# Optimization experiments

Measured on AMD Instinct MI355X. Metric: run time of the kernel, lower is better.

The kernel has to match this reference:

```python
import jax, jax.numpy as jnp
import numpy as np

B, TIN, TOUT = 64, 256, 400
NM, BF = 80, 512
MID, H, PRE = BF // 4, 2 * BF, BF // 2
LOC_F, LOC_K = 32, 31


def lstm_cell(x, h, c, Wih, Whh, bih, bhh):
    gates = x @ Wih.T + bih + h @ Whh.T + bhh
    i, f, g, o = jnp.split(gates, 4, axis=-1)
    c2 = jax.nn.sigmoid(f) * c + jax.nn.sigmoid(i) * jnp.tanh(g)
    h2 = jax.nn.sigmoid(o) * jnp.tanh(c2)
    return h2, c2


def setup_inputs() -> dict:
    key = jax.random.key(0)
    ks = jax.random.split(key, 24)
    def p(k, shape, fan_in):
        return jax.random.normal(k, shape, jnp.float32) / np.sqrt(fan_in)
    return {
        'input': jax.random.normal(ks[0], (B, TIN, BF), jnp.float32),
        'input_mask': jnp.ones((B, TIN), jnp.bool_),
        'target': jax.random.normal(ks[1], (B, NM, TOUT), jnp.float32),
        'W_pre1': p(ks[2], (PRE, NM), NM), 'b_pre1': jnp.zeros((PRE,), jnp.float32),
        'W_pre2': p(ks[3], (PRE, PRE), PRE), 'b_pre2': jnp.zeros((PRE,), jnp.float32),
        'Wq': p(ks[4], (MID, H), H),
        'Wk': p(ks[5], (MID, BF), BF),
        'loc_conv': p(ks[6], (LOC_F, 2, LOC_K), 2 * LOC_K),
        'Wloc': p(ks[7], (MID, LOC_F), LOC_F),
        'v_att': p(ks[8], (MID,), MID),
        'Wih1': p(ks[9], (4 * H, BF + PRE), BF + PRE), 'Whh1': p(ks[10], (4 * H, H), H),
        'bih1': jnp.zeros((4 * H,), jnp.float32), 'bhh1': jnp.zeros((4 * H,), jnp.float32),
        'Wih2': p(ks[11], (4 * H, BF + H), BF + H), 'Whh2': p(ks[12], (4 * H, H), H),
        'bih2': jnp.zeros((4 * H,), jnp.float32), 'bhh2': jnp.zeros((4 * H,), jnp.float32),
        'Wout': p(ks[13], (NM, BF + H), BF + H), 'bout': jnp.zeros((NM,), jnp.float32),
    }


def reference(input, input_mask, target, W_pre1, b_pre1, W_pre2, b_pre2, Wq, Wk,
              loc_conv, Wloc, v_att, Wih1, Whh1, bih1, bhh1, Wih2, Whh2, bih2, bhh2,
              Wout, bout):
    b, tin, f = input.shape
    nm, tout = target.shape[1], target.shape[2]
    # teacher-forcing shift: prepend zero frame, drop last
    tgt = jnp.concatenate([jnp.zeros((b, nm, 1), target.dtype), target[:, :, :-1]], 2)
    # PreNet: two 1x1 convs (== per-channel linears) + ReLU (dropout = eval identity)
    x = jax.nn.relu(jnp.einsum('bct,oc->bot', tgt, W_pre1) + b_pre1[None, :, None])
    x = jax.nn.relu(jnp.einsum('bct,oc->bot', x, W_pre2) + b_pre2[None, :, None])  # [B,PRE,Tout]
    key_proj = jnp.einsum('btf,mf->btm', input, Wk)  # [B,Tin,MID]
    pad = (LOC_K - 1) // 2

    def step(carry, xt):
        h1, c1, h2, c2, context, aw, awc = carry
        h1, c1 = lstm_cell(jnp.concatenate([xt, context], 1), h1, c1, Wih1, Whh1, bih1, bhh1)
        # location-sensitive attention
        wpair = jnp.stack([aw, awc], 1)  # [B,2,Tin]
        loc = jax.lax.conv_general_dilated(wpair, loc_conv, (1,), [(pad, pad)],
                                           dimension_numbers=('NCH', 'OIH', 'NCH'))
        loc_feat = jnp.einsum('bct,mc->btm', loc, Wloc)
        q = h1 @ Wq.T  # [B,MID]
        e = jnp.tanh(q[:, None, :] + key_proj + loc_feat) @ v_att  # [B,Tin]
        e = jnp.where(input_mask, e, jnp.float32(-1e9))
        aw2 = jax.nn.softmax(e, axis=1)
        context2 = jnp.einsum('bt,btf->bf', aw2, input)
        awc2 = awc + aw2
        h2, c2 = lstm_cell(jnp.concatenate([h1, context2], 1), h2, c2, Wih2, Whh2, bih2, bhh2)
        out = jnp.concatenate([h2, context2], 1) @ Wout.T + bout
        return (h1, c1, h2, c2, context2, aw2, awc2), (out, aw2)

    z = lambda *s: jnp.zeros(s, input.dtype)
    carry0 = (z(b, H), z(b, H), z(b, H), z(b, H), z(b, f), z(b, tin), z(b, tin))
    xs = jnp.transpose(x, (2, 0, 1))  # [Tout,B,PRE]
    _, (outs, aws) = jax.lax.scan(step, carry0, xs)
    output = jnp.moveaxis(outs, 0, 2)  # [B,NM,Tout]
    weight = jnp.moveaxis(aws, 0, 2)   # [B,Tin,Tout]
    return output, weight
```

## Files before the change

kernel.cpp:

```cpp
#include <hip/hip_runtime.h>

#define NB 256
#define NT 512
#define DYNB 158496
#define SCOPE __HIP_MEMORY_SCOPE_AGENT

typedef __attribute__((ext_vector_type(8))) short short8;
typedef __attribute__((ext_vector_type(4))) float f32x4;

__device__ __forceinline__ float b2f(unsigned short s){ return __uint_as_float(((unsigned)s)<<16); }
__device__ __forceinline__ unsigned short f2b(float f){
  unsigned u = __float_as_uint(f);
  return (unsigned short)((u + 0x7FFFu + ((u>>16)&1u))>>16);
}
__device__ __forceinline__ float sigm(float x){ return 1.0f/(1.0f+__expf(-x)); }
__device__ __forceinline__ float tanh_(float x){ float e=__expf(-2.0f*x); return (1.0f-e)/(1.0f+e); }
__device__ __forceinline__ f32x4 mfma16(short8 a, short8 b, f32x4 c){
  return __builtin_amdgcn_mfma_f32_16x16x32_bf16(a,b,c,0,0,0);
}

__device__ __forceinline__ unsigned long long ldu64(const void* p){
  return __hip_atomic_load((const unsigned long long*)p, __ATOMIC_RELAXED, SCOPE);
}
__device__ __forceinline__ short8 ld8h(const unsigned short* p){
  union{ unsigned long long u[2]; short8 s; } r;
  r.u[0]=ldu64(p); r.u[1]=ldu64(p+4);
  return r.s;
}
__device__ __forceinline__ float2 ld2f(const float* p){
  union{ unsigned long long u; float2 f; } r; r.u=ldu64(p); return r.f;
}
__device__ __forceinline__ float ldf(const float* p){
  return __hip_atomic_load((float*)p, __ATOMIC_RELAXED, SCOPE);
}
__device__ __forceinline__ void stf(float* p, float v){
  __hip_atomic_store(p, v, __ATOMIC_RELAXED, SCOPE);
}
__device__ __forceinline__ void sth(unsigned short* p, unsigned short v){
  __hip_atomic_store(p, v, __ATOMIC_RELAXED, SCOPE);
}

__device__ __forceinline__ void gbar2(unsigned* arrive, unsigned* root, unsigned* release,
                                      int grp, unsigned& ph){
  __syncthreads();
  if (threadIdx.x==0){
    ph += 1;
    asm volatile("s_waitcnt vmcnt(0)" ::: "memory");
    unsigned old = __hip_atomic_fetch_add(&arrive[grp*32], 1u, __ATOMIC_RELAXED, SCOPE);
    if (old == ph*32u - 1u){
      __hip_atomic_fetch_add(root, 1u, __ATOMIC_RELAXED, SCOPE);
      while (__hip_atomic_load(root, __ATOMIC_RELAXED, SCOPE) < ph*8u){
        __builtin_amdgcn_s_sleep(1);
      }
      __hip_atomic_store(&release[grp*32], ph, __ATOMIC_RELAXED, SCOPE);
    } else {
      while (__hip_atomic_load(&release[grp*32], __ATOMIC_RELAXED, SCOPE) < ph){
        __builtin_amdgcn_s_sleep(1);
      }
    }
  }
  __syncthreads();
}


__global__ void maskdet_k(const unsigned* __restrict__ m32, int* __restrict__ flag){
  __shared__ int ok;
  if (threadIdx.x==0) ok = 1;
  __syncthreads();
  for (int i=threadIdx.x; i<4096; i+=256){
    if (m32[i] > 1u) ok = 0;
  }
  __syncthreads();
  if (threadIdx.x==0) *flag = ok;
}

__global__ void xin2bf_k(const float* __restrict__ xin, unsigned short* __restrict__ xinh){
  size_t i = (size_t)blockIdx.x*256 + threadIdx.x;
  if (i < (size_t)64*256*512) xinh[i] = f2b(xin[i]);
}

__global__ void prenet_k(const float* __restrict__ target, const float* __restrict__ W1, const float* __restrict__ b1,
                         const float* __restrict__ W2, const float* __restrict__ b2,
                         unsigned short* __restrict__ xbh){
  int t = blockIdx.x;
  int tid = threadIdx.x;
  __shared__ float stgt[64][80];
  __shared__ float smid[64][256];
  for(int i=tid;i<64*80;i+=256){
    int b=i/80, c=i%80;
    stgt[b][c] = (t==0)?0.f : target[((size_t)b*80+c)*400 + (t-1)];
  }
  __syncthreads();
  {
    float w1r[80];
    #pragma unroll
    for(int c=0;c<80;c++) w1r[c] = W1[tid*80+c];
    float bb1 = b1[tid];
    for(int b0=0;b0<64;b0+=16){
      float acc[16];
      #pragma unroll
      for(int i=0;i<16;i++) acc[i]=0.f;
      for(int c=0;c<80;c++){
        float wv=w1r[c];
        #pragma unroll
        for(int i=0;i<16;i++) acc[i] += wv*stgt[b0+i][c];
      }
      #pragma unroll
      for(int i=0;i<16;i++) smid[b0+i][tid] = fmaxf(acc[i]+bb1, 0.f);
    }
  }
  __syncthreads();
  {
    float bb2 = b2[tid];
    for(int b0=0;b0<64;b0+=16){
      float acc[16];
      #pragma unroll
      for(int i=0;i<16;i++) acc[i]=0.f;
      for(int c=0;c<256;c++){
        float wv=W2[tid*256+c];
        #pragma unroll
        for(int i=0;i<16;i++) acc[i] += wv*smid[b0+i][c];
      }
      #pragma unroll
      for(int i=0;i<16;i++){
        float v = fmaxf(acc[i]+bb2,0.f);
        xbh[((size_t)t*64 + b0+i)*256 + tid] = f2b(v);
      }
    }
  }
}

__global__ void keyproj_k(const float* __restrict__ xin, const float* __restrict__ Wk, unsigned short* __restrict__ keypT){
  int b = blockIdx.x>>4; int t0=(blockIdx.x&15)*16; int m=threadIdx.x;
  __shared__ float sx[16][512];
  for(int i=m;i<16*512;i+=128){ int tt=i>>9, f=i&511; sx[tt][f]=xin[((size_t)b*256+t0+tt)*512+f]; }
  __syncthreads();
  float s[16];
  #pragma unroll
  for(int i=0;i<16;i++) s[i]=0.f;
  for(int f=0;f<512;f++){
    float wv = Wk[m*512+f];
    #pragma unroll
    for(int i=0;i<16;i++) s[i]+=sx[i][f]*wv;
  }
  #pragma unroll
  for(int i=0;i<16;i++) keypT[((size_t)b*128+m)*256 + t0+i] = f2b(s[i]);
}

__global__ void prep_k(const float* bih1,const float* bhh1,const float* bih2,const float* bhh2,
                       float* bsum1,float* bsum2){
  int i0 = blockIdx.x*blockDim.x + threadIdx.x;
  int n = gridDim.x*blockDim.x;
  for(int k=i0;k<4096;k+=n){ bsum1[k]=bih1[k]+bhh1[k]; bsum2[k]=bih2[k]+bhh2[k]; }
}

__global__ void perm_k(const float* __restrict__ Wih1, const float* __restrict__ Whh1,
                       const float* __restrict__ Wih2, const float* __restrict__ Whh2,
                       unsigned short* __restrict__ Wp1h, unsigned short* __restrict__ Wp2h){
  size_t i0 = (size_t)blockIdx.x*blockDim.x + threadIdx.x;
  size_t n  = (size_t)gridDim.x*blockDim.x;
  const size_t N1 = (size_t)256*56*512;
  for(size_t idx=i0; idx<N1; idx+=n){
    int beta = (int)(idx/28672);
    int r = (int)(idx%28672);
    int kt = r/512;
    int l  = (r>>3)&63;
    int i8 = r&7;
    int c = l&15, cci = l>>4;
    int k = kt*32 + cci*8 + i8;
    int rowp = (c>>2)*1024 + beta*4 + (c&3);
    float v = (k<768)? Wih1[(size_t)rowp*768 + k] : Whh1[(size_t)rowp*1024 + (k-768)];
    Wp1h[idx] = f2b(v);
  }
  const size_t N2 = (size_t)256*80*512;
  for(size_t idx=i0; idx<N2; idx+=n){
    int beta = (int)(idx/40960);
    int r = (int)(idx%40960);
    int kt = r/512;
    int l  = (r>>3)&63;
    int i8 = r&7;
    int c = l&15, cci = l>>4;
    int k = kt*32 + cci*8 + i8;
    int rowp = (c>>2)*1024 + beta*4 + (c&3);
    float v = (k<1536)? Wih2[(size_t)rowp*1536 + k] : Whh2[(size_t)rowp*1024 + (k-1536)];
    Wp2h[idx] = f2b(v);
  }
}


struct SArgs {
  const float* xin; const float* loc_conv; const float* Wloc; const float* v_att; const float* bout;
  const float* Wq; const float* Wout;
  const unsigned short* keypT; const unsigned short* xinh;
  const unsigned short* xbh;
  const unsigned short* Wp1h; const unsigned short* Wp2h;
  const float* bsum1; const float* bsum2;
  const unsigned char* mask8; const int* mask32; const int* mflag;
  unsigned short* h1h; float* h1f;
  unsigned short* h2h; float* h2f;
  unsigned short* ctxh; float* ctxf;
  float* c1; float* c2;
  float* aw; float* awc; float* eP; float* locT;
  unsigned* arrive; unsigned* root; unsigned* release;
  float* outp; float* wout;
};

__global__ void __launch_bounds__(NT) scan_kernel(SArgs a){
  extern __shared__ char dynsm[];
  unsigned short* Lw1 = (unsigned short*)dynsm;
  unsigned short* Lw2 = (unsigned short*)(dynsm + 57344);
  float* gsc1 = (float*)(dynsm + 139264);
  float* gsc2 = (float*)(dynsm + 143616);
  float* sA   = (float*)(dynsm + 147968);
  float* sq   = (float*)(dynsm + 158208);
  float* sv   = (float*)(dynsm + 158336);
  float* red  = (float*)(dynsm + 158464);

  const int beta = ((blockIdx.x & 7) << 5) | (blockIdx.x >> 3);
  const int grp  = blockIdx.x & 7;
  const int tid = threadIdx.x;
  const int wav = tid>>6;
  const int lan = tid&63;

  const int cc  = lan>>4;
  const int b4  = beta>>2;
  const int q4  = beta&3;
  unsigned ph = 0;

  {
    const short8* g1 = (const short8*)(a.Wp1h + (size_t)beta*28672);
    short8* l1 = (short8*)Lw1;
    for (int i=tid; i<3584; i+=NT) l1[i] = g1[i];
    const short8* g2 = (const short8*)(a.Wp2h + (size_t)beta*40960);
    short8* l2 = (short8*)Lw2;
    for (int i=tid; i<5120; i+=NT) l2[i] = g2[i];
  }

  bool mv = false;
  if (tid<256) mv = (a.mflag[0] ? (a.mask32[b4*256+tid] != 0) : (a.mask8[b4*256+tid] != 0));
  __syncthreads();

  for (int tau=0; tau<=400; ++tau){
    const int p = tau&1;
    if (tau<400 && wav<4){
      const int row = wav*16 + (lan&15);
      f32x4 A0={0.f,0.f,0.f,0.f};
      const unsigned short* wh = Lw1 + lan*8;
      {
        const unsigned short* xh = a.xbh + ((size_t)tau*64 + row)*256 + cc*8;
        #pragma unroll
        for(int kt=0;kt<8;kt++)
          A0=mfma16(*(const short8*)(xh+kt*32), *(const short8*)(wh+kt*512), A0);
      }
      {
        const unsigned short* xh = a.ctxh + row*512 + cc*8;
        #pragma unroll 8
        for(int kt=8;kt<24;kt++)
          A0=mfma16(ld8h(xh+(kt-8)*32), *(const short8*)(wh+kt*512), A0);
      }
      {
        const unsigned short* xh = a.h1h + (size_t)(p^1)*65536 + row*1024 + cc*8;
        #pragma unroll 8
        for(int kt=24;kt<56;kt++)
          A0=mfma16(ld8h(xh+(kt-24)*32), *(const short8*)(wh+kt*512), A0);
      }
      #pragma unroll
      for(int r=0;r<4;r++) gsc1[(wav*16 + cc*4 + r)*17 + (lan&15)] = A0[r];
    }
    if (tau>0 && wav>=4){
      const int wv2 = wav-4;
      const int row = wv2*16 + (lan&15);
      f32x4 A0={0.f,0.f,0.f,0.f};
      const unsigned short* wh = Lw2 + lan*8;
      {
        const unsigned short* xh = a.h1h + (size_t)(p^1)*65536 + row*1024 + cc*8;
        #pragma unroll 8
        for(int kt=0;kt<32;kt++)
          A0=mfma16(ld8h(xh+kt*32), *(const short8*)(wh+kt*512), A0);
      }
      {
        const unsigned short* xh = a.ctxh + row*512 + cc*8;
        #pragma unroll 8
        for(int kt=32;kt<48;kt++)
          A0=mfma16(ld8h(xh+(kt-32)*32), *(const short8*)(wh+kt*512), A0);
      }
      {
        const unsigned short* xh = a.h2h + (size_t)p*65536 + row*1024 + cc*8;
        #pragma unroll 8
        for(int kt=48;kt<80;kt++)
          A0=mfma16(ld8h(xh+(kt-48)*32), *(const short8*)(wh+kt*512), A0);
      }
      #pragma unroll
      for(int r=0;r<4;r++) gsc2[(wv2*16 + cc*4 + r)*17 + (lan&15)] = A0[r];
    }
    __syncthreads();
    if (tau<400 && tid<256){
      int m = tid>>2, j = tid&3, u = beta*4+j;
      float gi = gsc1[m*17+0+j]  + a.bsum1[0*1024+u];
      float gf = gsc1[m*17+4+j]  + a.bsum1[1*1024+u];
      float gg = gsc1[m*17+8+j]  + a.bsum1[2*1024+u];
      float go = gsc1[m*17+12+j] + a.bsum1[3*1024+u];
      float cp = a.c1[m*1024+u];
      float cn = sigm(gf)*cp + sigm(gi)*tanh_(gg);
      a.c1[m*1024+u] = cn;
      float hn = sigm(go)*tanh_(cn);
      stf(a.h1f + m*1024+u, hn);
      sth(a.h1h + (size_t)p*65536 + m*1024 + u, f2b(hn));
    }
    if (tau>0 && tid>=256){
      int t2 = tid-256;
      int m = t2>>2, j = t2&3, u = beta*4+j;
      float gi = gsc2[m*17+0+j]  + a.bsum2[0*1024+u];
      float gf = gsc2[m*17+4+j]  + a.bsum2[1*1024+u];
      float gg = gsc2[m*17+8+j]  + a.bsum2[2*1024+u];
      float go = gsc2[m*17+12+j] + a.bsum2[3*1024+u];
      float cp = a.c2[m*1024+u];
      float cn = sigm(gf)*cp + sigm(gi)*tanh_(gg);
      a.c2[m*1024+u] = cn;
      float hn = sigm(go)*tanh_(cn);
      stf(a.h2f + m*1024+u, hn);
      sth(a.h2h + (size_t)(p^1)*65536 + m*1024 + u, f2b(hn));
    }
    if (tau<400){
      if (tid<128){
        float2 v = ld2f(a.aw + b4*256 + tid*2);
        sA[tid*2]=v.x; sA[tid*2+1]=v.y;
        float2 w2 = ld2f(a.awc + b4*256 + tid*2);
        sA[256+tid*2]=w2.x; sA[257+tid*2]=w2.y;
      }
      for(int i=tid;i<1984;i+=NT) sA[512+i] = a.loc_conv[i];
    }
    __syncthreads();
    if (tau<400){
      const int t0 = q4*64;
      #pragma unroll
      for(int jj=0;jj<4;jj++){
        int o = tid*4+jj;
        int f = o>>6, tl = o&63, t = t0+tl;
        float s = 0.f;
        #pragma unroll
        for(int c=0;c<2;c++){
          const float* kw = &sA[512 + (f*2+c)*31];
          const float* wv = &sA[c*256];
          for(int k=0;k<31;k++){
            int tt = t + k - 15;
            if (tt>=0 && tt<256) s += wv[tt]*kw[k];
          }
        }
        stf(a.locT + (size_t)b4*8192 + f*256 + t, s);
      }
    }
    gbar2(a.arrive, a.root, a.release, grp, ph);
    if (tau<400 && tid<256){
      for(int i=tid*2;i<1024;i+=512){
        float2 v = ld2f(a.h1f + b4*1024 + i);
        sA[i]=v.x; sA[i+1]=v.y;
      }
    }
    if (tau>0 && tid>=256){
      int t2 = tid-256;
      for(int i=t2*2;i<1024;i+=512){
        float2 v = ld2f(a.h2f + b4*1024 + i);
        sA[1024+i]=v.x; sA[1025+i]=v.y;
      }
      {
        float2 v = ld2f(a.ctxf + b4*512 + t2*2);
        sA[2048+t2*2]=v.x; sA[2049+t2*2]=v.y;
      }
    }
    __syncthreads();
    if (tau<400 && tid<256){
      int ml = tid>>3, sg = tid&7;
      const float* wq = a.Wq + (size_t)(q4*32+ml)*1024;
      float s=0.f;
      #pragma unroll 8
      for(int i=0;i<128;i++) s += sA[sg + i*8]*wq[sg + i*8];
      s += __shfl_xor(s,1); s += __shfl_xor(s,2); s += __shfl_xor(s,4);
      if (sg==0) sq[ml] = s;
    }
    if (tau>0 && tid>=256 && tid<416){
      int t2 = tid-256;
      int nl = t2>>3, sg = t2&7, nm = q4*20+nl;
      const float* wo = a.Wout + (size_t)nm*1536;
      float s=0.f;
      #pragma unroll 8
      for(int i=0;i<192;i++) s += sA[1024 + sg + i*8]*wo[sg + i*8];
      s += __shfl_xor(s,1); s += __shfl_xor(s,2); s += __shfl_xor(s,4);
      if (sg==0) a.outp[(size_t)b4*32000 + nm*400 + (tau-1)] = s + a.bout[nm];
    }
    __syncthreads();
    if (tau<400 && tid<256){
      for(int i=tid;i<1024;i+=256) sA[i] = a.Wloc[(q4*32 + (i>>5))*32 + (i&31)];
    }
    if (tid<32) sv[tid] = a.v_att[q4*32+tid];
    __syncthreads();
    if (tau<400 && tid<256){
      int t = tid;
      float lc[32];
      const float* lb = a.locT + (size_t)b4*8192 + t;
      #pragma unroll
      for(int f=0;f<32;f++) lc[f] = ldf(lb + f*256);
      const unsigned short* kb = a.keypT + ((size_t)b4*128 + q4*32)*256 + t;
      float acc=0.f;
      for(int mm=0;mm<32;mm++){
        float lf=0.f;
        #pragma unroll
        for(int f=0;f<32;f++) lf += lc[f]*sA[mm*32+f];
        acc += tanh_(sq[mm] + b2f(kb[mm*256]) + lf)*sv[mm];
      }
      stf(a.eP + b4*1024 + t*4 + q4, acc);
    }
    if (tau==400) break;
    gbar2(a.arrive, a.root, a.release, grp, ph);
    {
      float e=0.f, pe=0.f, mx=0.f;
      if (tid<256){
        const float* ep = a.eP + b4*1024 + tid*4;
        e = ldf(ep+0)+ldf(ep+1)+ldf(ep+2)+ldf(ep+3);
        if (!mv) e = -1e9f;
        mx = e;
        #pragma unroll
        for(int off=1;off<64;off<<=1) mx = fmaxf(mx, __shfl_xor(mx,off));
        if (lan==0) red[wav] = mx;
      }
      __syncthreads();
      if (tid<256){
        mx = fmaxf(fmaxf(red[0],red[1]), fmaxf(red[2],red[3]));
        pe = __expf(e-mx);
        float sm = pe;
        #pragma unroll
        for(int off=1;off<64;off<<=1) sm += __shfl_xor(sm,off);
        if (lan==0) red[4+wav] = sm;
      }
      __syncthreads();
      if (tid<256){
        float sm = red[4]+red[5]+red[6]+red[7];
        float awt = pe/sm;
        if (q4==0){
          stf(a.aw + b4*256+tid, awt);
          stf(a.awc + b4*256+tid, ldf(a.awc + b4*256+tid) + awt);
          a.wout[(size_t)b4*102400 + (size_t)tid*400 + tau] = awt;
        }
        sA[tid] = awt;
      }
      __syncthreads();
      {
        int fl = tid&127, th = tid>>7;
        const unsigned short* xp = a.xinh + ((size_t)(b4*256 + th*64))*512 + q4*128 + fl;
        float s=0.f;
        for(int i=0;i<64;i++) s += sA[th*64+i]*b2f(xp[(size_t)i*512]);
        sA[256+tid] = s;
      }
      __syncthreads();
      if (tid<128){
        float v = sA[256+tid] + sA[384+tid] + sA[512+tid] + sA[640+tid];
        int idx = b4*512 + q4*128 + tid;
        stf(a.ctxf + idx, v);
        sth(a.ctxh + idx, f2b(v));
      }
    }
    gbar2(a.arrive, a.root, a.release, grp, ph);
  }
}

extern "C" void kernel_launch(void* const* d_in, const int* in_sizes, int n_in,
                              void* d_out, int out_size, void* d_ws, size_t ws_size,
                              hipStream_t stream){
  (void)in_sizes; (void)n_in; (void)out_size; (void)ws_size;
  const float* xin   = (const float*)d_in[0];
  const float* target= (const float*)d_in[2];
  const float* Wpre1 = (const float*)d_in[3];
  const float* bpre1 = (const float*)d_in[4];
  const float* Wpre2 = (const float*)d_in[5];
  const float* bpre2 = (const float*)d_in[6];
  const float* Wq    = (const float*)d_in[7];
  const float* Wk    = (const float*)d_in[8];
  const float* loc_conv = (const float*)d_in[9];
  const float* Wloc  = (const float*)d_in[10];
  const float* v_att = (const float*)d_in[11];
  const float* Wih1  = (const float*)d_in[12];
  const float* Whh1  = (const float*)d_in[13];
  const float* bih1  = (const float*)d_in[14];
  const float* bhh1  = (const float*)d_in[15];
  const float* Wih2  = (const float*)d_in[16];
  const float* Whh2  = (const float*)d_in[17];
  const float* bih2  = (const float*)d_in[18];
  const float* bhh2  = (const float*)d_in[19];
  const float* Wout  = (const float*)d_in[20];
  const float* boutp = (const float*)d_in[21];

  char* w = (char*)d_ws;
  auto carve=[&](size_t bytes)->void*{ void* r=(void*)w; w += (bytes+255)&~(size_t)255; return r; };
  unsigned short* h1h = (unsigned short*)carve((size_t)2*64*1024*2);
  unsigned short* h2h = (unsigned short*)carve((size_t)2*64*1024*2);
  unsigned short* ctxh= (unsigned short*)carve((size_t)64*512*2);
  float* h1f = (float*)carve((size_t)64*1024*4);
  float* h2f = (float*)carve((size_t)64*1024*4);
  float* ctxf= (float*)carve((size_t)64*512*4);
  float* c1  = (float*)carve((size_t)64*1024*4);
  float* c2  = (float*)carve((size_t)64*1024*4);
  float* aw  = (float*)carve((size_t)64*256*4);
  float* awc = (float*)carve((size_t)64*256*4);
  unsigned* arrive  = (unsigned*)carve(1024);
  unsigned* rootc   = (unsigned*)carve(256);
  unsigned* release = (unsigned*)carve(1024);
  int* mflag = (int*)carve(256);
  size_t state_bytes = (size_t)(w - (char*)d_ws);
  float* eP   = (float*)carve((size_t)64*256*4*4);
  float* locT = (float*)carve((size_t)64*32*256*4);
  unsigned short* keypT = (unsigned short*)carve((size_t)64*128*256*2);
  unsigned short* xinh  = (unsigned short*)carve((size_t)64*256*512*2);
  unsigned short* xbh = (unsigned short*)carve((size_t)400*64*256*2);
  float* bsum1 = (float*)carve((size_t)4096*4);
  float* bsum2 = (float*)carve((size_t)4096*4);
  unsigned short* Wp1h = (unsigned short*)carve((size_t)256*56*512*2);
  unsigned short* Wp2h = (unsigned short*)carve((size_t)256*80*512*2);

  hipMemsetAsync(d_ws, 0, state_bytes, stream);
  maskdet_k<<<1, 256, 0, stream>>>((const unsigned*)d_in[1], mflag);
  xin2bf_k<<<32768, 256, 0, stream>>>(xin, xinh);
  prenet_k<<<400, 256, 0, stream>>>(target, Wpre1, bpre1, Wpre2, bpre2, xbh);
  keyproj_k<<<1024, 128, 0, stream>>>(xin, Wk, keypT);
  prep_k<<<16, 256, 0, stream>>>(bih1,bhh1,bih2,bhh2,bsum1,bsum2);
  perm_k<<<2048, 256, 0, stream>>>(Wih1,Whh1,Wih2,Whh2,Wp1h,Wp2h);

  SArgs a;
  a.xin=xin; a.loc_conv=loc_conv; a.Wloc=Wloc; a.v_att=v_att; a.bout=boutp;
  a.Wq=Wq; a.Wout=Wout;
  a.keypT=keypT; a.xinh=xinh; a.xbh=xbh;
  a.Wp1h=Wp1h; a.Wp2h=Wp2h;
  a.bsum1=bsum1; a.bsum2=bsum2;
  a.mask8=(const unsigned char*)d_in[1]; a.mask32=(const int*)d_in[1]; a.mflag=mflag;
  a.h1h=h1h; a.h1f=h1f;
  a.h2h=h2h; a.h2f=h2f;
  a.ctxh=ctxh; a.ctxf=ctxf;
  a.c1=c1; a.c2=c2;
  a.aw=aw; a.awc=awc; a.eP=eP; a.locT=locT;
  a.arrive=arrive; a.root=rootc; a.release=release;
  a.outp=(float*)d_out; a.wout=(float*)d_out + (size_t)64*80*400;

  hipFuncSetAttribute((const void*)scan_kernel, hipFuncAttributeMaxDynamicSharedMemorySize, DYNB);
  scan_kernel<<<dim3(NB), dim3(NT), DYNB, stream>>>(a);
}
```

Baseline: 51.29 ms.

## Use per-timestep rotating state buffers so recurrent loads can be plain cached loads

Replaces the double-buffered h1/h2/ctx state with per-timestep write-once buffers (400 slots each), so every read location is written exactly once and plain non-atomic vector loads can replace the relaxed atomic 64-bit loads in the MFMA input streams. It also drops the fp32 copies of h1, h2 and the context and rebuilds the shared-memory fp32 values from the bf16 copies. The aim is to cut L2-coherent atomic load overhead and duplicate fp32 stores on the critical recurrent path. In exchange it uses much more workspace, touches a fresh address range every step, and feeds bf16-rounded values into the attention and output paths that used fp32 before.

```diff
diff --git a/kernel.cpp b/kernel.cpp
--- a/kernel.cpp
+++ b/kernel.cpp
@@ -19,16 +19,10 @@
   return __builtin_amdgcn_mfma_f32_16x16x32_bf16(a,b,c,0,0,0);
 }
 
-__device__ __forceinline__ unsigned long long ldu64(const void* p){
-  return __hip_atomic_load((const unsigned long long*)p, __ATOMIC_RELAXED, SCOPE);
-}
-__device__ __forceinline__ short8 ld8h(const unsigned short* p){
-  union{ unsigned long long u[2]; short8 s; } r;
-  r.u[0]=ldu64(p); r.u[1]=ldu64(p+4);
-  return r.s;
-}
 __device__ __forceinline__ float2 ld2f(const float* p){
-  union{ unsigned long long u; float2 f; } r; r.u=ldu64(p); return r.f;
+  union{ unsigned long long u; float2 f; } r;
+  r.u = __hip_atomic_load((const unsigned long long*)p, __ATOMIC_RELAXED, SCOPE);
+  return r.f;
 }
 __device__ __forceinline__ float ldf(const float* p){
   return __hip_atomic_load((float*)p, __ATOMIC_RELAXED, SCOPE);
@@ -189,16 +183,15 @@
 
 
 struct SArgs {
-  const float* xin; const float* loc_conv; const float* Wloc; const float* v_att; const float* bout;
-  const float* Wq; const float* Wout;
+  const float* loc_conv; const float* v_att; const float* bout;
+  const float* Wq; const float* Wout; const float* Wloc;
   const unsigned short* keypT; const unsigned short* xinh;
   const unsigned short* xbh;
   const unsigned short* Wp1h; const unsigned short* Wp2h;
   const float* bsum1; const float* bsum2;
   const unsigned char* mask8; const int* mask32; const int* mflag;
-  unsigned short* h1h; float* h1f;
-  unsigned short* h2h; float* h2f;
-  unsigned short* ctxh; float* ctxf;
+  unsigned short* h1rot; unsigned short* h2rot; unsigned short* ctxrot;
+  const unsigned short* zbuf;
   float* c1; float* c2;
   float* aw; float* awc; float* eP; float* locT;
   unsigned* arrive; unsigned* root; unsigned* release;
@@ -241,7 +234,13 @@
   __syncthreads();
 
   for (int tau=0; tau<=400; ++tau){
-    const int p = tau&1;
+    const unsigned short* h1p = (tau==0)? a.zbuf : a.h1rot + (size_t)(tau-1)*65536;
+    const unsigned short* h2p = (tau<=1)? a.zbuf : a.h2rot + (size_t)(tau-2)*65536;
+    const unsigned short* cxp = (tau==0)? a.zbuf : a.ctxrot + (size_t)(tau-1)*32768;
+    unsigned short* h1w = a.h1rot + (size_t)tau*65536;
+    unsigned short* h2w = a.h2rot + (size_t)(tau>0 ? tau-1 : 0)*65536;
+    unsigned short* cxw = a.ctxrot + (size_t)tau*32768;
+
     if (tau<400 && wav<4){
       const int row = wav*16 + (lan&15);
       f32x4 A0={0.f,0.f,0.f,0.f};
@@ -253,16 +252,16 @@
           A0=mfma16(*(const short8*)(xh+kt*32), *(const short8*)(wh+kt*512), A0);
       }
       {
-        const unsigned short* xh = a.ctxh + row*512 + cc*8;
+        const unsigned short* xh = cxp + row*512 + cc*8;
         #pragma unroll 8
         for(int kt=8;kt<24;kt++)
-          A0=mfma16(ld8h(xh+(kt-8)*32), *(const short8*)(wh+kt*512), A0);
-      }
-      {
-        const unsigned short* xh = a.h1h + (size_t)(p^1)*65536 + row*1024 + cc*8;
+          A0=mfma16(*(const short8*)(xh+(kt-8)*32), *(const short8*)(wh+kt*512), A0);
+      }
+      {
+        const unsigned short* xh = h1p + row*1024 + cc*8;
         #pragma unroll 8
         for(int kt=24;kt<56;kt++)
-          A0=mfma16(ld8h(xh+(kt-24)*32), *(const short8*)(wh+kt*512), A0);
+          A0=mfma16(*(const short8*)(xh+(kt-24)*32), *(const short8*)(wh+kt*512), A0);
       }
       #pragma unroll
       for(int r=0;r<4;r++) gsc1[(wav*16 + cc*4 + r)*17 + (lan&15)] = A0[r];
@@ -273,22 +272,22 @@
       f32x4 A0={0.f,0.f,0.f,0.f};
       const unsigned short* wh = Lw2 + lan*8;
       {
-        const unsigned short* xh = a.h1h + (size_t)(p^1)*65536 + row*1024 + cc*8;
+        const unsigned short* xh = h1p + row*1024 + cc*8;
         #pragma unroll 8
         for(int kt=0;kt<32;kt++)
-          A0=mfma16(ld8h(xh+kt*32), *(const short8*)(wh+kt*512), A0);
-      }
-      {
-        const unsigned short* xh = a.ctxh + row*512 + cc*8;
+          A0=mfma16(*(const short8*)(xh+kt*32), *(const short8*)(wh+kt*512), A0);
+      }
+      {
+        const unsigned short* xh = cxp + row*512 + cc*8;
         #pragma unroll 8
         for(int kt=32;kt<48;kt++)
-          A0=mfma16(ld8h(xh+(kt-32)*32), *(const short8*)(wh+kt*512), A0);
-      }
-      {
-        const unsigned short* xh = a.h2h + (size_t)p*65536 + row*1024 + cc*8;
+          A0=mfma16(*(const short8*)(xh+(kt-32)*32), *(const short8*)(wh+kt*512), A0);
+      }
+      {
+        const unsigned short* xh = h2p + row*1024 + cc*8;
         #pragma unroll 8
         for(int kt=48;kt<80;kt++)
-          A0=mfma16(ld8h(xh+(kt-48)*32), *(const short8*)(wh+kt*512), A0);
+          A0=mfma16(*(const short8*)(xh+(kt-48)*32), *(const short8*)(wh+kt*512), A0);
       }
       #pragma unroll
       for(int r=0;r<4;r++) gsc2[(wv2*16 + cc*4 + r)*17 + (lan&15)] = A0[r];
@@ -304,8 +303,7 @@
       float cn = sigm(gf)*cp + sigm(gi)*tanh_(gg);
       a.c1[m*1024+u] = cn;
       float hn = sigm(go)*tanh_(cn);
-      stf(a.h1f + m*1024+u, hn);
-      sth(a.h1h + (size_t)p*65536 + m*1024 + u, f2b(hn));
+      sth(h1w + m*1024 + u, f2b(hn));
     }
     if (tau>0 && tid>=256){
       int t2 = tid-256;
@@ -318,8 +316,7 @@
       float cn = sigm(gf)*cp + sigm(gi)*tanh_(gg);
       a.c2[m*1024+u] = cn;
       float hn = sigm(go)*tanh_(cn);
-      stf(a.h2f + m*1024+u, hn);
-      sth(a.h2h + (size_t)(p^1)*65536 + m*1024 + u, f2b(hn));
+      sth(h2w + m*1024 + u, f2b(hn));
     }
     if (tau<400){
       if (tid<128){
@@ -352,21 +349,15 @@
     }
     gbar2(a.arrive, a.root, a.release, grp, ph);
     if (tau<400 && tid<256){
-      for(int i=tid*2;i<1024;i+=512){
-        float2 v = ld2f(a.h1f + b4*1024 + i);
-        sA[i]=v.x; sA[i+1]=v.y;
-      }
+      const unsigned short* h1c = a.h1rot + (size_t)tau*65536 + b4*1024;
+      for(int i=tid;i<1024;i+=256) sA[i] = b2f(h1c[i]);
     }
     if (tau>0 && tid>=256){
       int t2 = tid-256;
-      for(int i=t2*2;i<1024;i+=512){
-        float2 v = ld2f(a.h2f + b4*1024 + i);
-        sA[1024+i]=v.x; sA[1025+i]=v.y;
-      }
-      {
-        float2 v = ld2f(a.ctxf + b4*512 + t2*2);
-        sA[2048+t2*2]=v.x; sA[2049+t2*2]=v.y;
-      }
+      const unsigned short* h2c = a.h2rot + (size_t)(tau-1)*65536 + b4*1024;
+      const unsigned short* cxc = a.ctxrot + (size_t)(tau-1)*32768 + b4*512;
+      for(int i=t2;i<1024;i+=256) sA[1024+i] = b2f(h2c[i]);
+      for(int i=t2;i<512;i+=256)  sA[2048+i] = b2f(cxc[i]);
     }
     __syncthreads();
     if (tau<400 && tid<256){
@@ -454,9 +445,7 @@
       __syncthreads();
       if (tid<128){
         float v = sA[256+tid] + sA[384+tid] + sA[512+tid] + sA[640+tid];
-        int idx = b4*512 + q4*128 + tid;
-        stf(a.ctxf + idx, v);
-        sth(a.ctxh + idx, f2b(v));
+        sth(cxw + b4*512 + q4*128 + tid, f2b(v));
       }
     }
     gbar2(a.arrive, a.root, a.release, grp, ph);
@@ -491,12 +480,7 @@
 
   char* w = (char*)d_ws;
   auto carve=[&](size_t bytes)->void*{ void* r=(void*)w; w += (bytes+255)&~(size_t)255; return r; };
-  unsigned short* h1h = (unsigned short*)carve((size_t)2*64*1024*2);
-  unsigned short* h2h = (unsigned short*)carve((size_t)2*64*1024*2);
-  unsigned short* ctxh= (unsigned short*)carve((size_t)64*512*2);
-  float* h1f = (float*)carve((size_t)64*1024*4);
-  float* h2f = (float*)carve((size_t)64*1024*4);
-  float* ctxf= (float*)carve((size_t)64*512*4);
+  unsigned short* zbuf = (unsigned short*)carve((size_t)64*1024*2);
   float* c1  = (float*)carve((size_t)64*1024*4);
   float* c2  = (float*)carve((size_t)64*1024*4);
   float* aw  = (float*)carve((size_t)64*256*4);
@@ -515,6 +499,9 @@
   float* bsum2 = (float*)carve((size_t)4096*4);
   unsigned short* Wp1h = (unsigned short*)carve((size_t)256*56*512*2);
   unsigned short* Wp2h = (unsigned short*)carve((size_t)256*80*512*2);
+  unsigned short* h1rot = (unsigned short*)carve((size_t)400*65536*2);
+  unsigned short* h2rot = (unsigned short*)carve((size_t)400*65536*2);
+  unsigned short* ctxrot= (unsigned short*)carve((size_t)400*32768*2);
 
   hipMemsetAsync(d_ws, 0, state_bytes, stream);
   maskdet_k<<<1, 256, 0, stream>>>((const unsigned*)d_in[1], mflag);
@@ -525,15 +512,13 @@
   perm_k<<<2048, 256, 0, stream>>>(Wih1,Whh1,Wih2,Whh2,Wp1h,Wp2h);
 
   SArgs a;
-  a.xin=xin; a.loc_conv=loc_conv; a.Wloc=Wloc; a.v_att=v_att; a.bout=boutp;
-  a.Wq=Wq; a.Wout=Wout;
+  a.loc_conv=loc_conv; a.v_att=v_att; a.bout=boutp;
+  a.Wq=Wq; a.Wout=Wout; a.Wloc=Wloc;
   a.keypT=keypT; a.xinh=xinh; a.xbh=xbh;
   a.Wp1h=Wp1h; a.Wp2h=Wp2h;
   a.bsum1=bsum1; a.bsum2=bsum2;
   a.mask8=(const unsigned char*)d_in[1]; a.mask32=(const int*)d_in[1]; a.mflag=mflag;
-  a.h1h=h1h; a.h1f=h1f;
-  a.h2h=h2h; a.h2f=h2f;
-  a.ctxh=ctxh; a.ctxf=ctxf;
+  a.h1rot=h1rot; a.h2rot=h2rot; a.ctxrot=ctxrot; a.zbuf=zbuf;
   a.c1=c1; a.c2=c2;
   a.aw=aw; a.awc=awc; a.eP=eP; a.locT=locT;
   a.arrive=arrive; a.root=rootc; a.release=release;
```

Result: faster. 46.80 ms (-8.8%).
